# Optimization experiments

Hardware: AMD Instinct MI355X
Metric: run time of the kernel (lower is better)

## Reference

```python
import jax, jax.numpy as jnp
import numpy as np

B, S, D = 32, 1024, 1024   # batch, seq_len, d_model
P, F = 4, 4096             # num_phases, d_ff
# Each phase owns a contiguous split of S/P sequence positions (set_splits builds
# a disjoint contiguous partition of the sequence; assert t == seq_length).


def setup_inputs() -> dict:
    key = jax.random.key(0)
    ks = jax.random.split(key, 6)
    x = jax.random.normal(ks[0], (B, S, D), dtype=jnp.float32)
    phases = jax.random.randint(ks[1], (B, S), 0, P, dtype=jnp.int32)
    s1 = 1.0 / np.sqrt(D)
    s2 = 1.0 / np.sqrt(F)
    W1 = jax.random.uniform(ks[2], (P, D, F), jnp.float32, -s1, s1)
    b1 = jax.random.uniform(ks[3], (P, F), jnp.float32, -s1, s1)
    W2 = jax.random.uniform(ks[4], (P, F, D), jnp.float32, -s2, s2)
    b2 = jax.random.uniform(ks[5], (P, D), jnp.float32, -s2, s2)
    return {"x": x, "W1": W1, "b1": b1, "W2": W2, "b2": b2, "phases": phases}


def reference(x, W1, b1, W2, b2, phases):
    # Branched path (phases.ndim > 1): gather each phase's contiguous split,
    # run that phase's FF, scatter back. Since the static phase_mask is a
    # contiguous equal partition, gather/scatter == reshape into [B, P, S/P, D].
    xs = x.reshape(B, P, S // P, D)
    h = jax.nn.relu(jnp.einsum('bpsd,pdf->bpsf', xs, W1) + b1[None, :, None, :])
    y = jnp.einsum('bpsf,pfd->bpsd', h, W2) + b2[None, :, None, :]
    return y.reshape(B, S, D)
```

## Files before the change

kernel.cpp:

```cpp
#include <hip/hip_runtime.h>
#include <hip/hip_bf16.h>
#include <stdint.h>

typedef __bf16 bf16_t;
typedef bf16_t bf16x8 __attribute__((ext_vector_type(8)));
typedef bf16_t bf16x4 __attribute__((ext_vector_type(4)));
typedef float  f32x4  __attribute__((ext_vector_type(4)));

#define AS1(p) ((const __attribute__((address_space(1))) void*)(p))
#define AS3(p) ((__attribute__((address_space(3))) void*)(p))

static constexpr int B_ = 32, S_ = 1024, D_ = 1024, P_ = 4, F_ = 4096;
static constexpr int SPP = S_ / P_;
static constexpr int MP  = B_ * SPP;

__global__ void conv_x_kernel(const float* __restrict__ x, bf16_t* __restrict__ xg) {
  const int64_t n4 = (int64_t)B_ * S_ * D_ / 4;
  for (int64_t i = (int64_t)blockIdx.x * blockDim.x + threadIdx.x; i < n4;
       i += (int64_t)gridDim.x * blockDim.x) {
    int64_t e = i << 2;
    int d = (int)(e & (D_ - 1));
    int s = (int)((e >> 10) & (S_ - 1));
    int b = (int)(e >> 20);
    int p = s >> 8;
    int r = (b << 8) | (s & 255);
    const float4 v = ((const float4*)x)[i];
    bf16x4 o;
    o[0] = (bf16_t)v.x; o[1] = (bf16_t)v.y; o[2] = (bf16_t)v.z; o[3] = (bf16_t)v.w;
    *(bf16x4*)&xg[(((int64_t)p * MP + r) << 10) | d] = o;
  }
}

__global__ void conv_wt_kernel(const float* __restrict__ W, bf16_t* __restrict__ Wt,
                               int K, int N) {
  __shared__ bf16_t tile[32][33];
  const int p = blockIdx.z;
  const float* Wp = W + (int64_t)p * K * N;
  bf16_t* Wtp = Wt + (int64_t)p * K * N;
  const int n0 = blockIdx.x * 32, k0 = blockIdx.y * 32;
  const int tx = threadIdx.x & 31, ty = threadIdx.x >> 5;
  #pragma unroll
  for (int j = 0; j < 4; ++j) {
    int kr = ty + j * 8;
    tile[kr][tx] = (bf16_t)Wp[(int64_t)(k0 + kr) * N + n0 + tx];
  }
  __syncthreads();
  #pragma unroll
  for (int j = 0; j < 4; ++j) {
    int nr = ty + j * 8;
    Wtp[(int64_t)(n0 + nr) * K + k0 + tx] = tile[tx][nr];
  }
}


__device__ __forceinline__ bf16x8 ldsfrag(const char* region, int row, int cb) {
  return *(const bf16x8*)(region + row * 128 + (cb ^ ((row & 7) << 4)));
}

template<int LDK>
__device__ __forceinline__ void stage_half(const bf16_t* gsrc, char* ldsreg, int t) {
  #pragma unroll
  for (int j = 0; j < 2; ++j) {
    const int idx = j * 512 + t;
    const int row = idx >> 3;
    const int cb  = ((idx & 7) << 4) ^ ((row & 7) << 4);
    __builtin_amdgcn_global_load_lds(AS1((const char*)(gsrc + (int64_t)row * LDK) + cb),
                                     AS3(ldsreg + idx * 16), 16, 0, 0);
  }
}

#define MFMA_QUAD(AF, BF, MO, NO) \
  do { _Pragma("unroll") for (int m_ = 0; m_ < 4; ++m_) \
       _Pragma("unroll") for (int n_ = 0; n_ < 2; ++n_) \
       _Pragma("unroll") for (int k_ = 0; k_ < 2; ++k_) \
         acc[(MO) + m_][(NO) + n_] = __builtin_amdgcn_mfma_f32_16x16x32_bf16( \
             AF[m_][k_], BF[n_][k_], acc[(MO) + m_][(NO) + n_], 0, 0, 0); } while (0)

#define READ_A4(DST, REG, MO) \
  do { _Pragma("unroll") for (int m_ = 0; m_ < 4; ++m_) \
       _Pragma("unroll") for (int k_ = 0; k_ < 2; ++k_) \
         DST[m_][k_] = ldsfrag(REG, wm * 128 + ((MO) + m_) * 16 + fr, k_ * 64 + hi * 16); } while (0)

#define READ_B2(DST, REG, NO) \
  do { _Pragma("unroll") for (int n_ = 0; n_ < 2; ++n_) \
       _Pragma("unroll") for (int k_ = 0; k_ < 2; ++k_) \
         DST[n_][k_] = ldsfrag(REG, wn * 64 + ((NO) + n_) * 16 + fr, k_ * 64 + hi * 16); } while (0)

#define BAR()   __builtin_amdgcn_s_barrier()
#define SBAR()  __builtin_amdgcn_sched_barrier(0)
#define PRIO(x) __builtin_amdgcn_s_setprio(x)
#define VMCNT6() asm volatile("s_waitcnt vmcnt(6)" ::: "memory")
#define VMCNT0() asm volatile("s_waitcnt vmcnt(0)" ::: "memory")

template<bool RELU, bool OUT_BF16, int KK, int NN>
__global__ __launch_bounds__(512, 2)
void ffgemm8_kernel(const bf16_t* __restrict__ A, const bf16_t* __restrict__ Bt,
                    const float* __restrict__ bias, void* __restrict__ outv, int M) {
  static_assert(KK % 128 == 0, "need even number of 64-wide K tiles");
  __shared__ __align__(16) char smem[131072];
  char* const At0 = smem;
  char* const At1 = smem + 32768;
  char* const Bs0 = smem + 65536;
  char* const Bs1 = smem + 98304;

  const int t = threadIdx.x, lane = t & 63, w = t >> 6;
  const int wm = w >> 2, wn = w & 3;
  const int fr = lane & 15, hi = lane >> 4;

  const int gx = gridDim.x, gy = gridDim.y;
  const int nwg = gx * gy * (int)gridDim.z;
  const int id  = ((int)blockIdx.z * gy + (int)blockIdx.y) * gx + (int)blockIdx.x;
  const int swz = (id & 7) * (nwg >> 3) + (id >> 3);
  const int bx = swz % gx;
  const int rem = swz / gx;
  const int by = rem % gy;
  const int p  = rem / gy;

  const int tile_m = by * 256, tile_n = bx * 256;
  const bf16_t* Ab = A  + (int64_t)p * M  * KK + (int64_t)tile_m * KK;
  const bf16_t* Bb = Bt + (int64_t)p * NN * KK + (int64_t)tile_n * KK;
  const float* biasp = bias + (int64_t)p * NN;

  f32x4 acc[8][4] = {};
  constexpr int NT = KK / 64, NI = NT / 2;

  stage_half<KK>(Ab,                        At0,          t);
  stage_half<KK>(Ab + (int64_t)128 * KK,    At0 + 16384,  t);
  stage_half<KK>(Bb,                        Bs0,          t);
  stage_half<KK>(Bb + (int64_t)128 * KK,    Bs0 + 16384,  t);
  stage_half<KK>(Bb + 64,                   Bs1,          t);
  stage_half<KK>(Bb + (int64_t)128 * KK + 64, Bs1 + 16384, t);
  stage_half<KK>(Ab + 64,                   At1,          t);
  VMCNT6();
  BAR(); SBAR();

  for (int i = 0; i < NI; ++i) {
    const int k0 = i * 128;
    const bool more = (i < NI - 1);
    bf16x8 a0[4][2], a1[4][2], b0[2][2], b1[2][2];

    READ_A4(a0, At0, 0); READ_B2(b0, Bs0, 0);
    stage_half<KK>(Ab + (int64_t)128 * KK + (k0 + 64), At1 + 16384, t);
    BAR(); PRIO(1); MFMA_QUAD(a0, b0, 0, 0); PRIO(0); BAR();
    READ_B2(b1, Bs0, 2);
    if (more) stage_half<KK>(Bb + (k0 + 128), Bs0, t);
    BAR(); PRIO(1); MFMA_QUAD(a0, b1, 0, 2); PRIO(0); BAR();
    READ_A4(a1, At0, 4);
    if (more) stage_half<KK>(Bb + (int64_t)128 * KK + (k0 + 128), Bs0 + 16384, t);
    BAR(); PRIO(1); MFMA_QUAD(a1, b0, 4, 0); PRIO(0); BAR();
    if (more) stage_half<KK>(Ab + (k0 + 128), At0, t);
    BAR(); PRIO(1); MFMA_QUAD(a1, b1, 4, 2); PRIO(0);
    if (more) VMCNT6(); else VMCNT0();
    BAR(); SBAR();

    READ_A4(a0, At1, 0); READ_B2(b0, Bs1, 0);
    if (more) stage_half<KK>(Ab + (int64_t)128 * KK + (k0 + 128), At0 + 16384, t);
    BAR(); PRIO(1); MFMA_QUAD(a0, b0, 0, 0); PRIO(0); BAR();
    READ_B2(b1, Bs1, 2);
    if (more) stage_half<KK>(Bb + (k0 + 192), Bs1, t);
    BAR(); PRIO(1); MFMA_QUAD(a0, b1, 0, 2); PRIO(0); BAR();
    READ_A4(a1, At1, 4);
    if (more) stage_half<KK>(Bb + (int64_t)128 * KK + (k0 + 192), Bs1 + 16384, t);
    BAR(); PRIO(1); MFMA_QUAD(a1, b0, 4, 0); PRIO(0); BAR();
    if (more) stage_half<KK>(Ab + (k0 + 192), At1, t);
    BAR(); PRIO(1); MFMA_QUAD(a1, b1, 4, 2); PRIO(0);
    if (more) VMCNT6(); else VMCNT0();
    BAR(); SBAR();
  }

  float bv[4];
  #pragma unroll
  for (int n = 0; n < 4; ++n) bv[n] = biasp[tile_n + wn * 64 + n * 16 + fr];
  if (OUT_BF16) {
    bf16_t* out = (bf16_t*)outv + (int64_t)p * M * NN;
    #pragma unroll
    for (int m = 0; m < 8; ++m)
      #pragma unroll
      for (int j = 0; j < 4; ++j) {
        const int row = tile_m + wm * 128 + m * 16 + hi * 4 + j;
        #pragma unroll
        for (int n = 0; n < 4; ++n) {
          const int col = tile_n + wn * 64 + n * 16 + fr;
          float v = acc[m][n][j] + bv[n];
          if (RELU) v = fmaxf(v, 0.0f);
          out[(int64_t)row * NN + col] = (bf16_t)v;
        }
      }
  } else {
    float* out = (float*)outv;
    #pragma unroll
    for (int m = 0; m < 8; ++m)
      #pragma unroll
      for (int j = 0; j < 4; ++j) {
        const int row = tile_m + wm * 128 + m * 16 + hi * 4 + j;
        const int grow = ((row >> 8) << 10) + p * SPP + (row & 255);
        #pragma unroll
        for (int n = 0; n < 4; ++n) {
          const int col = tile_n + wn * 64 + n * 16 + fr;
          out[(int64_t)grow * NN + col] = acc[m][n][j] + bv[n];
        }
      }
  }
}

extern "C" void kernel_launch(void* const* d_in, const int* in_sizes, int n_in,
                              void* d_out, int out_size, void* d_ws, size_t ws_size,
                              hipStream_t stream) {
  (void)in_sizes; (void)n_in; (void)out_size; (void)ws_size;
  const float* x  = (const float*)d_in[0];
  const float* W1 = (const float*)d_in[1];
  const float* b1 = (const float*)d_in[2];
  const float* W2 = (const float*)d_in[3];
  const float* b2 = (const float*)d_in[4];
  float* y = (float*)d_out;

  char* ws = (char*)d_ws;
  bf16_t* xg = (bf16_t*)ws;
  bf16_t* wt = (bf16_t*)(ws + (size_t)64 * 1024 * 1024);
  bf16_t* h  = (bf16_t*)(ws + (size_t)96 * 1024 * 1024);

  conv_x_kernel<<<2048, 256, 0, stream>>>(x, xg);
  conv_wt_kernel<<<dim3(F_ / 32, D_ / 32, P_), 256, 0, stream>>>(W1, wt, D_, F_);
  ffgemm8_kernel<true, true, 1024, 4096><<<dim3(F_ / 256, MP / 256, P_), 512, 0, stream>>>(
      xg, wt, b1, h, MP);
  conv_wt_kernel<<<dim3(D_ / 32, F_ / 32, P_), 256, 0, stream>>>(W2, wt, F_, D_);
  ffgemm8_kernel<false, false, 4096, 1024><<<dim3(D_ / 256, MP / 256, P_), 512, 0, stream>>>(
      h, wt, b2, y, MP);
}
```

Measured before the change: 579.0 us.

## Rework LDS wait placement, regroup B staging, and band-swizzle tile order

Adds explicit lgkmcnt waits (partial before the barrier, full after) so each MFMA quad waits on exactly its LDS fragment reads. Moves both halves of the next B tile's global-to-LDS staging into a single slot after the last B fragment read. Also changes the workgroup-to-tile mapping to walk bands of four M tiles across N within each phase, aiming at better L2 reuse. The heavier waits and the changed staging order could expose LDS latency or alter the number of outstanding loads that VMCNT6 assumes.

```diff
diff --git a/kernel.cpp b/kernel.cpp
--- a/kernel.cpp
+++ b/kernel.cpp
@@ -91,6 +91,8 @@
 #define PRIO(x) __builtin_amdgcn_s_setprio(x)
 #define VMCNT6() asm volatile("s_waitcnt vmcnt(6)" ::: "memory")
 #define VMCNT0() asm volatile("s_waitcnt vmcnt(0)" ::: "memory")
+#define LGKM0() do { asm volatile("s_waitcnt lgkmcnt(0)" ::: "memory"); SBAR(); } while (0)
+#define LGKM8() asm volatile("s_waitcnt lgkmcnt(8)" ::: "memory")
 
 template<bool RELU, bool OUT_BF16, int KK, int NN>
 __global__ __launch_bounds__(512, 2)
@@ -111,10 +113,11 @@
   const int nwg = gx * gy * (int)gridDim.z;
   const int id  = ((int)blockIdx.z * gy + (int)blockIdx.y) * gx + (int)blockIdx.x;
   const int swz = (id & 7) * (nwg >> 3) + (id >> 3);
-  const int bx = swz % gx;
-  const int rem = swz / gx;
-  const int by = rem % gy;
-  const int p  = rem / gy;
+  const int per_p = gx * gy;
+  const int p  = swz / per_p;
+  const int q  = swz % per_p;
+  const int band = q / (gx * 4), qq = q % (gx * 4);
+  const int bx = qq >> 2, by = band * 4 + (qq & 3);
 
   const int tile_m = by * 256, tile_n = bx * 256;
   const bf16_t* Ab = A  + (int64_t)p * M  * KK + (int64_t)tile_m * KK;
@@ -122,15 +125,15 @@
   const float* biasp = bias + (int64_t)p * NN;
 
   f32x4 acc[8][4] = {};
-  constexpr int NT = KK / 64, NI = NT / 2;
-
-  stage_half<KK>(Ab,                        At0,          t);
-  stage_half<KK>(Ab + (int64_t)128 * KK,    At0 + 16384,  t);
-  stage_half<KK>(Bb,                        Bs0,          t);
-  stage_half<KK>(Bb + (int64_t)128 * KK,    Bs0 + 16384,  t);
-  stage_half<KK>(Bb + 64,                   Bs1,          t);
-  stage_half<KK>(Bb + (int64_t)128 * KK + 64, Bs1 + 16384, t);
-  stage_half<KK>(Ab + 64,                   At1,          t);
+  constexpr int NI = KK / 128;
+
+  stage_half<KK>(Ab,                          At0,          t);
+  stage_half<KK>(Ab + (int64_t)128 * KK,      At0 + 16384,  t);
+  stage_half<KK>(Bb,                          Bs0,          t);
+  stage_half<KK>(Bb + (int64_t)128 * KK,      Bs0 + 16384,  t);
+  stage_half<KK>(Bb + 64,                     Bs1,          t);
+  stage_half<KK>(Bb + (int64_t)128 * KK + 64, Bs1 + 16384,  t);
+  stage_half<KK>(Ab + 64,                     At1,          t);
   VMCNT6();
   BAR(); SBAR();
 
@@ -141,29 +144,29 @@
 
     READ_A4(a0, At0, 0); READ_B2(b0, Bs0, 0);
     stage_half<KK>(Ab + (int64_t)128 * KK + (k0 + 64), At1 + 16384, t);
-    BAR(); PRIO(1); MFMA_QUAD(a0, b0, 0, 0); PRIO(0); BAR();
+    LGKM8(); BAR(); LGKM0(); PRIO(1); MFMA_QUAD(a0, b0, 0, 0); PRIO(0); BAR();
     READ_B2(b1, Bs0, 2);
-    if (more) stage_half<KK>(Bb + (k0 + 128), Bs0, t);
-    BAR(); PRIO(1); MFMA_QUAD(a0, b1, 0, 2); PRIO(0); BAR();
+    BAR(); LGKM0(); PRIO(1); MFMA_QUAD(a0, b1, 0, 2); PRIO(0); BAR();
     READ_A4(a1, At0, 4);
-    if (more) stage_half<KK>(Bb + (int64_t)128 * KK + (k0 + 128), Bs0 + 16384, t);
-    BAR(); PRIO(1); MFMA_QUAD(a1, b0, 4, 0); PRIO(0); BAR();
+    if (more) { stage_half<KK>(Bb + (k0 + 128), Bs0, t);
+                stage_half<KK>(Bb + (int64_t)128 * KK + (k0 + 128), Bs0 + 16384, t); }
+    BAR(); LGKM0(); PRIO(1); MFMA_QUAD(a1, b0, 4, 0); PRIO(0); BAR();
     if (more) stage_half<KK>(Ab + (k0 + 128), At0, t);
-    BAR(); PRIO(1); MFMA_QUAD(a1, b1, 4, 2); PRIO(0);
+    BAR(); LGKM0(); PRIO(1); MFMA_QUAD(a1, b1, 4, 2); PRIO(0);
     if (more) VMCNT6(); else VMCNT0();
     BAR(); SBAR();
 
     READ_A4(a0, At1, 0); READ_B2(b0, Bs1, 0);
     if (more) stage_half<KK>(Ab + (int64_t)128 * KK + (k0 + 128), At0 + 16384, t);
-    BAR(); PRIO(1); MFMA_QUAD(a0, b0, 0, 0); PRIO(0); BAR();
+    LGKM8(); BAR(); LGKM0(); PRIO(1); MFMA_QUAD(a0, b0, 0, 0); PRIO(0); BAR();
     READ_B2(b1, Bs1, 2);
-    if (more) stage_half<KK>(Bb + (k0 + 192), Bs1, t);
-    BAR(); PRIO(1); MFMA_QUAD(a0, b1, 0, 2); PRIO(0); BAR();
+    BAR(); LGKM0(); PRIO(1); MFMA_QUAD(a0, b1, 0, 2); PRIO(0); BAR();
     READ_A4(a1, At1, 4);
-    if (more) stage_half<KK>(Bb + (int64_t)128 * KK + (k0 + 192), Bs1 + 16384, t);
-    BAR(); PRIO(1); MFMA_QUAD(a1, b0, 4, 0); PRIO(0); BAR();
+    if (more) { stage_half<KK>(Bb + (k0 + 192), Bs1, t);
+                stage_half<KK>(Bb + (int64_t)128 * KK + (k0 + 192), Bs1 + 16384, t); }
+    BAR(); LGKM0(); PRIO(1); MFMA_QUAD(a1, b0, 4, 0); PRIO(0); BAR();
     if (more) stage_half<KK>(Ab + (k0 + 192), At1, t);
-    BAR(); PRIO(1); MFMA_QUAD(a1, b1, 4, 2); PRIO(0);
+    BAR(); LGKM0(); PRIO(1); MFMA_QUAD(a1, b1, 4, 2); PRIO(0);
     if (more) VMCNT6(); else VMCNT0();
     BAR(); SBAR();
   }
```

New measurement: 575.1 us. Within noise of the previous version (-0.7%).
